# Kernel tuning notes

Hardware: AMD Instinct MI355X
Metric: run time of the kernel (lower is better)

The kernel has to match this reference:

```python
import jax, jax.numpy as jnp
import numpy as np

DIM = 384
HEADS = 8


def _dwconv3x3(x, w):
    # depthwise 3x3, groups = channels, padding=1 (SAME)
    return jax.lax.conv_general_dilated(
        x, w, window_strides=(1, 1), padding='SAME',
        feature_group_count=x.shape[1],
        dimension_numbers=('NCHW', 'OIHW', 'NCHW'))


def _conv1x1(x, w):
    return jax.lax.conv_general_dilated(
        x, w, window_strides=(1, 1), padding='SAME',
        dimension_numbers=('NCHW', 'OIHW', 'NCHW'))


def setup_inputs() -> dict:
    key = jax.random.key(0)
    ks = jax.random.split(key, 7)
    b, h, w = 2, 128, 128
    f = lambda k, s: jax.random.normal(k, s, dtype=jnp.float32)
    return {
        'k_fea': f(ks[0], (b, DIM, h, w)),
        'v_fea': f(ks[1], (b, DIM, h, w)),
        'q_fea': f(ks[2], (b, DIM, h, w)),
        'wq': f(ks[3], (DIM, 1, 3, 3)) * 0.1,
        'wk': f(ks[4], (DIM, 1, 3, 3)) * 0.1,
        'wv': f(ks[5], (DIM, 1, 3, 3)) * 0.1,
        'wproj': f(ks[6], (DIM, DIM, 1, 1)) * 0.05,
        'temperature': jnp.ones((HEADS, 1, 1), jnp.float32),
        'attn_w': jnp.full((4,), 0.2, jnp.float32),  # attn1..attn4 scalars
    }


def reference(k_fea, v_fea, q_fea, wq, wk, wv, wproj, temperature, attn_w):
    b, c, h, w = q_fea.shape
    q = _dwconv3x3(q_fea, wq)
    k = _dwconv3x3(k_fea, wk)
    v = _dwconv3x3(v_fea, wv)
    hw = h * w
    C = c // HEADS  # channels per head
    rs = lambda t: t.reshape(b, HEADS, C, hw)
    q, k, v = rs(q), rs(k), rs(v)
    # F.normalize(dim=-1): L2 normalize with eps clamp
    norm = lambda t: t / jnp.maximum(
        jnp.linalg.norm(t, axis=-1, keepdims=True), 1e-12)
    q, k = norm(q), norm(k)
    # channel-channel attention [b, heads, C, C]
    attn = jnp.einsum('bhcn,bhdn->bhcd', q, k) * temperature
    ar = jnp.arange(C)
    neg_inf = jnp.float32(-jnp.inf)
    ks_list = [C // 2, C * 2 // 3, C * 3 // 4, C * 4 // 5]
    out = jnp.zeros((b, HEADS, C, hw), attn.dtype)
    for i, topk in enumerate(ks_list):
        idx = jax.lax.top_k(attn, topk)[1]          # [b,h,C,topk]
        mask = (idx[..., None] == ar).any(axis=-2)  # [b,h,C,C] bool
        a = jax.nn.softmax(jnp.where(mask, attn, neg_inf), axis=-1)
        out = out + attn_w[i] * jnp.einsum('bhcd,bhdn->bhcn', a, v)
    out = out.reshape(b, c, h, w)
    return _conv1x1(out, wproj)
```

## Files before the change

kernel.cpp:

```cpp
#include <hip/hip_runtime.h>
#include <stdint.h>

#define NB 2
#define CH 384
#define NH 8
#define CPH 48
#define IMG 128
#define HW 16384

typedef float f32x4 __attribute__((ext_vector_type(4)));
typedef short bf16x8 __attribute__((ext_vector_type(8)));
typedef short short4v __attribute__((ext_vector_type(4)));

__device__ inline unsigned short f2bf(float f){
    unsigned u = __builtin_bit_cast(unsigned, f);
    u += 0x7FFFu + ((u >> 16) & 1u);
    return (unsigned short)(u >> 16);
}
__device__ inline float bf2f(unsigned short h){
    unsigned u = ((unsigned)h) << 16;
    return __builtin_bit_cast(float, u);
}

__device__ __forceinline__ void conv8(const float* __restrict__ pl,
                                      const float* w9, int x, int y, float* o)
{
#pragma unroll
    for (int j = 0; j < 8; ++j) o[j] = 0.f;
#pragma unroll
    for (int dy = 0; dy < 3; ++dy) {
        const int yy = y + dy - 1;
        const float vm = (yy >= 0 && yy < IMG) ? 1.f : 0.f;
        const int yc = yy < 0 ? 0 : (yy > IMG - 1 ? IMG - 1 : yy);
        const float* row = pl + yc * IMG;
        float4 A  = *(const float4*)(row + x);
        float4 Bv = *(const float4*)(row + x + 4);
        float lf = (x > 0)       ? row[x - 1] * vm : 0.f;
        float rt = (x < IMG - 8) ? row[x + 8] * vm : 0.f;
        A.x *= vm; A.y *= vm; A.z *= vm; A.w *= vm;
        Bv.x *= vm; Bv.y *= vm; Bv.z *= vm; Bv.w *= vm;
        const float a0 = w9[dy * 3], a1 = w9[dy * 3 + 1], a2 = w9[dy * 3 + 2];
        o[0] += a0 * lf   + a1 * A.x  + a2 * A.y;
        o[1] += a0 * A.x  + a1 * A.y  + a2 * A.z;
        o[2] += a0 * A.y  + a1 * A.z  + a2 * A.w;
        o[3] += a0 * A.z  + a1 * A.w  + a2 * Bv.x;
        o[4] += a0 * A.w  + a1 * Bv.x + a2 * Bv.y;
        o[5] += a0 * Bv.x + a1 * Bv.y + a2 * Bv.z;
        o[6] += a0 * Bv.y + a1 * Bv.z + a2 * Bv.w;
        o[7] += a0 * Bv.z + a1 * Bv.w + a2 * rt;
    }
}

__device__ __forceinline__ void packhl(const float* o, bf16x8& hi, bf16x8& lo,
                                       float& sq)
{
#pragma unroll
    for (int j = 0; j < 8; ++j) {
        sq += o[j] * o[j];
        unsigned short hh = f2bf(o[j]);
        hi[j] = (short)hh;
        lo[j] = (short)f2bf(o[j] - bf2f(hh));
    }
}

__global__ __launch_bounds__(256) void k_gramf(
    const float* __restrict__ qf, const float* __restrict__ kf,
    const float* __restrict__ wq, const float* __restrict__ wk,
    float* __restrict__ Sg, float* __restrict__ ssqg)
{
    __shared__ float sred[4][2304];
    __shared__ float ssr[4][96];
    const int t = threadIdx.x;
    const int s = blockIdx.x, bh = blockIdx.y;
    const int wid = t >> 6, lane = t & 63, quad = lane >> 4, l15 = lane & 15;
    const int b = bh >> 3, h = bh & 7;
    const int y = s * 4 + wid;

    const float* qpl[3];
    const float* kpl[3];
    float wqr[3][9], wkr[3][9];
#pragma unroll
    for (int i = 0; i < 3; ++i) {
        const int c = h * CPH + i * 16 + l15;
        qpl[i] = qf + (size_t)(b * CH + c) * HW;
        kpl[i] = kf + (size_t)(b * CH + c) * HW;
#pragma unroll
        for (int j = 0; j < 9; ++j) {
            wqr[i][j] = wq[c * 9 + j];
            wkr[i][j] = wk[c * 9 + j];
        }
    }

    f32x4 acc[3][3];
#pragma unroll
    for (int i = 0; i < 3; ++i)
#pragma unroll
        for (int j = 0; j < 3; ++j) acc[i][j] = (f32x4){0.f, 0.f, 0.f, 0.f};
    float sqq[3] = {0.f, 0.f, 0.f}, sqk[3] = {0.f, 0.f, 0.f};

    for (int ks = 0; ks < 4; ++ks) {
        const int x = ks * 32 + quad * 8;
        bf16x8 qh[3], ql_[3], kh[3], kl[3];
#pragma unroll
        for (int i = 0; i < 3; ++i) {
            float o[8];
            conv8(qpl[i], wqr[i], x, y, o);
            packhl(o, qh[i], ql_[i], sqq[i]);
            conv8(kpl[i], wkr[i], x, y, o);
            packhl(o, kh[i], kl[i], sqk[i]);
        }
#pragma unroll
        for (int ci = 0; ci < 3; ++ci)
#pragma unroll
            for (int di = 0; di < 3; ++di) {
                acc[ci][di] = __builtin_amdgcn_mfma_f32_16x16x32_bf16(qh[ci],  kh[di], acc[ci][di], 0, 0, 0);
                acc[ci][di] = __builtin_amdgcn_mfma_f32_16x16x32_bf16(qh[ci],  kl[di], acc[ci][di], 0, 0, 0);
                acc[ci][di] = __builtin_amdgcn_mfma_f32_16x16x32_bf16(ql_[ci], kh[di], acc[ci][di], 0, 0, 0);
            }
    }

#pragma unroll
    for (int i = 0; i < 3; ++i) {
#pragma unroll
        for (int off = 16; off <= 32; off <<= 1) {
            sqq[i] += __shfl_xor(sqq[i], off);
            sqk[i] += __shfl_xor(sqk[i], off);
        }
        if (lane < 16) {
            ssr[wid][i * 16 + l15]      = sqq[i];
            ssr[wid][48 + i * 16 + l15] = sqk[i];
        }
    }

#pragma unroll
    for (int ci = 0; ci < 3; ++ci)
#pragma unroll
        for (int di = 0; di < 3; ++di)
#pragma unroll
            for (int r = 0; r < 4; ++r)
                sred[wid][(ci * 16 + quad * 4 + r) * 48 + di * 16 + l15] = acc[ci][di][r];
    __syncthreads();

    if (t < 96)
        atomicAdd(&ssqg[(size_t)bh * 96 + t],
                  ssr[0][t] + ssr[1][t] + ssr[2][t] + ssr[3][t]);

    float* Sbh = Sg + (size_t)bh * 2304;
#pragma unroll
    for (int i = 0; i < 9; ++i) {
        int e = t * 9 + i;
        atomicAdd(&Sbh[e], sred[0][e] + sred[1][e] + sred[2][e] + sred[3][e]);
    }
}

__global__ __launch_bounds__(256) void k_conv3v(
    const float* __restrict__ vf, const float* __restrict__ wv,
    unsigned short* __restrict__ Vc)
{
    const int bc = blockIdx.x;
    const int ch = bc % CH;
    const float* plane = vf + (size_t)bc * HW;
    const float* wp9 = wv + ch * 9;
    unsigned short* oh = Vc + (size_t)bc * HW;

    float w9[9];
#pragma unroll
    for (int i = 0; i < 9; ++i) w9[i] = wp9[i];

    const int t = threadIdx.x;
    const int wvid = t >> 6, lane = t & 63;
    const int rb = lane >> 5, cx = lane & 31;

    for (int pass = 0; pass < 16; ++pass) {
        const int y = wvid * 32 + pass * 2 + rb;
        float o0 = 0.f, o1 = 0.f, o2 = 0.f, o3 = 0.f;
#pragma unroll
        for (int dy = 0; dy < 3; ++dy) {
            const int yy = y + dy - 1;
            const float vm = (yy >= 0 && yy < IMG) ? 1.f : 0.f;
            const int yc = yy < 0 ? 0 : (yy > IMG - 1 ? IMG - 1 : yy);
            float4 r4 = *(const float4*)(plane + yc * IMG + 4 * cx);
            r4.x *= vm; r4.y *= vm; r4.z *= vm; r4.w *= vm;
            float lf = __shfl(r4.w, (lane + 63) & 63);
            if (cx == 0) lf = 0.f;
            float rt = __shfl(r4.x, (lane + 1) & 63);
            if (cx == 31) rt = 0.f;
            const float a0 = w9[dy * 3], a1 = w9[dy * 3 + 1], a2 = w9[dy * 3 + 2];
            o0 += a0 * lf   + a1 * r4.x + a2 * r4.y;
            o1 += a0 * r4.x + a1 * r4.y + a2 * r4.z;
            o2 += a0 * r4.y + a1 * r4.z + a2 * r4.w;
            o3 += a0 * r4.z + a1 * r4.w + a2 * rt;
        }
        short4v pv = {(short)f2bf(o0), (short)f2bf(o1), (short)f2bf(o2), (short)f2bf(o3)};
        *(short4v*)(oh + y * IMG + 4 * cx) = pv;
    }
}

__global__ void k_attn(const float* __restrict__ Sg, const float* __restrict__ ssqg,
                       const float* __restrict__ temp, const float* __restrict__ aw,
                       float* __restrict__ Mg)
{
    const int t = threadIdx.x;
    const int r = blockIdx.x * 4 + (t >> 6);
    const int lane = t & 63;
    const int c = r % 48, h = (r / 48) % NH, b = r / (48 * NH);
    const float* Srow = Sg + ((size_t)(b * NH + h) * 48 + c) * 48;
    const float* sq = ssqg + (size_t)(b * NH + h) * 96;

    float v = -3.0e38f;
    if (lane < 48) {
        float nq = fmaxf(sqrtf(sq[c]), 1e-12f);
        float nk = fmaxf(sqrtf(sq[48 + lane]), 1e-12f);
        v = Srow[lane] / (nq * nk) * temp[h];
    }
    float m = v;
#pragma unroll
    for (int off = 32; off; off >>= 1) m = fmaxf(m, __shfl_xor(m, off));
    int rank = 0;
    for (int e = 0; e < 48; ++e) {
        float ve = __shfl(v, e);
        rank += ((ve > v) || (ve == v && e < lane)) ? 1 : 0;
    }
    float ed = (lane < 48) ? __expf(v - m) : 0.f;
    const int K4[4] = {24, 32, 36, 38};
    float f = 0.f;
#pragma unroll
    for (int i = 0; i < 4; ++i) {
        float x = (rank < K4[i]) ? ed : 0.f;
#pragma unroll
        for (int off = 32; off; off >>= 1) x += __shfl_xor(x, off);
        if (rank < K4[i]) f += aw[i] / x;
    }
    if (lane < 48) Mg[((size_t)(b * NH + h) * 48 + c) * 48 + lane] = ed * f;
}

__global__ void k_w2(const float* __restrict__ wproj, const float* __restrict__ Mg,
                     unsigned short* __restrict__ W2)
{
    int idx = blockIdx.x * 256 + threadIdx.x;
    int gd = idx % 384; int co = (idx / 384) % 384; int b = idx / (384 * 384);
    int h = gd / 48, d = gd % 48;
    const float* wp = wproj + (size_t)co * 384 + h * 48;
    const float* Mp = Mg + (size_t)(b * NH + h) * 2304 + d;
    float s = 0.f;
#pragma unroll
    for (int cc = 0; cc < 48; ++cc) s += wp[cc] * Mp[cc * 48];
    W2[idx] = f2bf(s);
}

__global__ __launch_bounds__(256) void k_trans(const unsigned short* __restrict__ Vc,
                                               unsigned short* __restrict__ Vct)
{
    __shared__ unsigned short S[64][66];
    const int nt = blockIdx.x, ct = blockIdx.y, b = blockIdx.z;
    const int t = threadIdx.x, r = t >> 2, seg = t & 3;
    const unsigned short* src = Vc + (size_t)(b * CH + ct * 64 + r) * HW + nt * 64 + seg * 16;
    *(bf16x8*)&S[r][seg * 16]     = *(const bf16x8*)src;
    *(bf16x8*)&S[r][seg * 16 + 8] = *(const bf16x8*)(src + 8);
    __syncthreads();
    unsigned short tmp[16];
#pragma unroll
    for (int i = 0; i < 16; ++i) tmp[i] = S[seg * 16 + i][r];
    unsigned short* dst = Vct + ((size_t)b * HW + nt * 64 + r) * CH + ct * 64 + seg * 16;
    *(bf16x8*)dst       = *(const bf16x8*)&tmp[0];
    *(bf16x8*)(dst + 8) = *(const bf16x8*)&tmp[8];
}

__global__ __launch_bounds__(256) void k_gemm2(const unsigned short* __restrict__ W2,
        const unsigned short* __restrict__ Vct, float* __restrict__ out)
{
    const int t = threadIdx.x;
    const int y = blockIdx.x, mt = blockIdx.y, b = blockIdx.z;
    const int wid = t >> 6, lane = t & 63, quad = lane >> 4, l15 = lane & 15;
    const int wm = wid >> 1, wn = wid & 1;

    f32x4 acc[4][4];
#pragma unroll
    for (int i = 0; i < 4; ++i)
#pragma unroll
        for (int j = 0; j < 4; ++j) acc[i][j] = (f32x4){0.f, 0.f, 0.f, 0.f};

    const unsigned short* Ab[4];
    const unsigned short* Bb[4];
#pragma unroll
    for (int i = 0; i < 4; ++i) {
        Ab[i] = W2 + (size_t)(b * CH + mt * 128 + wm * 64 + i * 16 + l15) * CH + quad * 8;
        Bb[i] = Vct + ((size_t)b * HW + y * IMG + wn * 64 + i * 16 + l15) * CH + quad * 8;
    }

    for (int kt = 0; kt < 12; ++kt) {
        const int K0 = kt * 32;
        bf16x8 af[4], bfr[4];
#pragma unroll
        for (int i = 0; i < 4; ++i) af[i]  = *(const bf16x8*)(Ab[i] + K0);
#pragma unroll
        for (int i = 0; i < 4; ++i) bfr[i] = *(const bf16x8*)(Bb[i] + K0);
#pragma unroll
        for (int mi = 0; mi < 4; ++mi)
#pragma unroll
            for (int ni = 0; ni < 4; ++ni)
                acc[mi][ni] = __builtin_amdgcn_mfma_f32_16x16x32_bf16(af[mi], bfr[ni], acc[mi][ni], 0, 0, 0);
    }
#pragma unroll
    for (int mi = 0; mi < 4; ++mi)
#pragma unroll
        for (int ni = 0; ni < 4; ++ni)
#pragma unroll
            for (int r = 0; r < 4; ++r) {
                int co = mt * 128 + wm * 64 + mi * 16 + quad * 4 + r;
                int n  = y * IMG + wn * 64 + ni * 16 + l15;
                out[(size_t)(b * CH + co) * HW + n] = acc[mi][ni][r];
            }
}

extern "C" void kernel_launch(void* const* d_in, const int* in_sizes, int n_in,
                              void* d_out, int out_size, void* d_ws, size_t ws_size,
                              hipStream_t stream)
{
    const float* k_fea = (const float*)d_in[0];
    const float* v_fea = (const float*)d_in[1];
    const float* q_fea = (const float*)d_in[2];
    const float* wq = (const float*)d_in[3];
    const float* wk = (const float*)d_in[4];
    const float* wv = (const float*)d_in[5];
    const float* wproj = (const float*)d_in[6];
    const float* temp = (const float*)d_in[7];
    const float* aw = (const float*)d_in[8];
    float* out = (float*)d_out;

    char* ws = (char*)d_ws;
    float* Sg   = (float*)ws;
    float* ssqg = (float*)(ws + 147456);
    float* Mg   = (float*)(ws + 153600);
    unsigned short* W2 = (unsigned short*)(ws + 301056);

    const size_t PLANE_BYTES = (size_t)NB * CH * HW * 2;
    unsigned short* Vc  = (unsigned short*)(ws + 890880);
    unsigned short* Vct = (unsigned short*)(ws + 890880 + PLANE_BYTES);

    hipMemsetAsync(Sg, 0, 153600, stream);
    k_conv3v<<<768, 256, 0, stream>>>(v_fea, wv, Vc);
    k_gramf<<<dim3(32, 16), 256, 0, stream>>>(q_fea, k_fea, wq, wk, Sg, ssqg);
    k_attn<<<192, 256, 0, stream>>>(Sg, ssqg, temp, aw, Mg);
    k_w2<<<1152, 256, 0, stream>>>(wproj, Mg, W2);
    k_trans<<<dim3(256, 6, 2), 256, 0, stream>>>(Vc, Vct);
    k_gemm2<<<dim3(128, 3, 2), 256, 0, stream>>>(W2, Vct, out);
}
```

Baseline: 378.6 us.

## Restructure Gram kernel to stage conv outputs in LDS with coalesced row loads

The fused q/k depthwise-conv plus Gram kernel now has each 16-lane group compute a full image row of one channel with coalesced float4 loads. Left and right halo values come from lane shuffles instead of extra scalar loads. The bf16 hi/lo results are written to XOR-swizzled shared memory and then read back in MFMA operand layout. Weights are cached in LDS, and the grid doubles to 64 blocks per head, with two rows per block and a 3-blocks-per-CU occupancy hint. The aim is better global-memory coalescing and occupancy, at the cost of extra LDS traffic, barriers per row, and twice as many atomic reductions into the Gram matrix.

```diff
diff --git a/kernel.cpp b/kernel.cpp
--- a/kernel.cpp
+++ b/kernel.cpp
@@ -22,35 +22,6 @@
     return __builtin_bit_cast(float, u);
 }
 
-__device__ __forceinline__ void conv8(const float* __restrict__ pl,
-                                      const float* w9, int x, int y, float* o)
-{
-#pragma unroll
-    for (int j = 0; j < 8; ++j) o[j] = 0.f;
-#pragma unroll
-    for (int dy = 0; dy < 3; ++dy) {
-        const int yy = y + dy - 1;
-        const float vm = (yy >= 0 && yy < IMG) ? 1.f : 0.f;
-        const int yc = yy < 0 ? 0 : (yy > IMG - 1 ? IMG - 1 : yy);
-        const float* row = pl + yc * IMG;
-        float4 A  = *(const float4*)(row + x);
-        float4 Bv = *(const float4*)(row + x + 4);
-        float lf = (x > 0)       ? row[x - 1] * vm : 0.f;
-        float rt = (x < IMG - 8) ? row[x + 8] * vm : 0.f;
-        A.x *= vm; A.y *= vm; A.z *= vm; A.w *= vm;
-        Bv.x *= vm; Bv.y *= vm; Bv.z *= vm; Bv.w *= vm;
-        const float a0 = w9[dy * 3], a1 = w9[dy * 3 + 1], a2 = w9[dy * 3 + 2];
-        o[0] += a0 * lf   + a1 * A.x  + a2 * A.y;
-        o[1] += a0 * A.x  + a1 * A.y  + a2 * A.z;
-        o[2] += a0 * A.y  + a1 * A.z  + a2 * A.w;
-        o[3] += a0 * A.z  + a1 * A.w  + a2 * Bv.x;
-        o[4] += a0 * A.w  + a1 * Bv.x + a2 * Bv.y;
-        o[5] += a0 * Bv.x + a1 * Bv.y + a2 * Bv.z;
-        o[6] += a0 * Bv.y + a1 * Bv.z + a2 * Bv.w;
-        o[7] += a0 * Bv.z + a1 * Bv.w + a2 * rt;
-    }
-}
-
 __device__ __forceinline__ void packhl(const float* o, bf16x8& hi, bf16x8& lo,
                                        float& sq)
 {
@@ -63,93 +34,129 @@
     }
 }
 
-__global__ __launch_bounds__(256) void k_gramf(
+__global__ __launch_bounds__(256, 3) void k_gramf2(
     const float* __restrict__ qf, const float* __restrict__ kf,
     const float* __restrict__ wq, const float* __restrict__ wk,
     float* __restrict__ Sg, float* __restrict__ ssqg)
 {
-    __shared__ float sred[4][2304];
-    __shared__ float ssr[4][96];
+    __shared__ char smem[49152];
+    __shared__ float ssqL[96];
+    __shared__ float wL[864];
+
     const int t = threadIdx.x;
     const int s = blockIdx.x, bh = blockIdx.y;
     const int wid = t >> 6, lane = t & 63, quad = lane >> 4, l15 = lane & 15;
     const int b = bh >> 3, h = bh & 7;
-    const int y = s * 4 + wid;
-
-    const float* qpl[3];
-    const float* kpl[3];
-    float wqr[3][9], wkr[3][9];
-#pragma unroll
-    for (int i = 0; i < 3; ++i) {
-        const int c = h * CPH + i * 16 + l15;
-        qpl[i] = qf + (size_t)(b * CH + c) * HW;
-        kpl[i] = kf + (size_t)(b * CH + c) * HW;
-#pragma unroll
-        for (int j = 0; j < 9; ++j) {
-            wqr[i][j] = wq[c * 9 + j];
-            wkr[i][j] = wk[c * 9 + j];
+
+    for (int idx = t; idx < 864; idx += 256)
+        wL[idx] = (idx < 432) ? wq[h * 432 + idx] : wk[h * 432 + idx - 432];
+    if (t < 96) ssqL[t] = 0.f;
+
+    f32x4 acc[3][3];
+#pragma unroll
+    for (int i = 0; i < 3; ++i)
+#pragma unroll
+        for (int j = 0; j < 3; ++j) acc[i][j] = (f32x4){0.f, 0.f, 0.f, 0.f};
+
+    const int xg = t & 15;
+    const int grp = t >> 4;
+
+    __syncthreads();
+
+    for (int r = 0; r < 2; ++r) {
+        const int y = s * 2 + r;
+
+#pragma unroll
+        for (int it = 0; it < 6; ++it) {
+            const int tc = it * 16 + grp;
+            const int tensor = tc >= 48 ? 1 : 0;
+            const int ch = tc - tensor * 48;
+            const float* pl = (tensor ? kf : qf) + (size_t)(b * CH + h * CPH + ch) * HW;
+            const float* wp = &wL[tensor * 432 + ch * 9];
+
+            float o[8];
+#pragma unroll
+            for (int j = 0; j < 8; ++j) o[j] = 0.f;
+#pragma unroll
+            for (int dy = 0; dy < 3; ++dy) {
+                const int yy = y + dy - 1;
+                const float vm = (yy >= 0 && yy < IMG) ? 1.f : 0.f;
+                const int yc = yy < 0 ? 0 : (yy > IMG - 1 ? IMG - 1 : yy);
+                const float* row = pl + yc * IMG + xg * 8;
+                float4 A  = *(const float4*)row;
+                float4 Bv = *(const float4*)(row + 4);
+                A.x *= vm; A.y *= vm; A.z *= vm; A.w *= vm;
+                Bv.x *= vm; Bv.y *= vm; Bv.z *= vm; Bv.w *= vm;
+                float lf = __shfl(Bv.w, (lane + 63) & 63);
+                if (xg == 0) lf = 0.f;
+                float rt = __shfl(A.x, (lane + 1) & 63);
+                if (xg == 15) rt = 0.f;
+                const float a0 = wp[dy * 3], a1 = wp[dy * 3 + 1], a2 = wp[dy * 3 + 2];
+                o[0] += a0 * lf   + a1 * A.x  + a2 * A.y;
+                o[1] += a0 * A.x  + a1 * A.y  + a2 * A.z;
+                o[2] += a0 * A.y  + a1 * A.z  + a2 * A.w;
+                o[3] += a0 * A.z  + a1 * A.w  + a2 * Bv.x;
+                o[4] += a0 * A.w  + a1 * Bv.x + a2 * Bv.y;
+                o[5] += a0 * Bv.x + a1 * Bv.y + a2 * Bv.z;
+                o[6] += a0 * Bv.y + a1 * Bv.z + a2 * Bv.w;
+                o[7] += a0 * Bv.z + a1 * Bv.w + a2 * rt;
+            }
+            float sq = 0.f;
+            bf16x8 hi, lo;
+            packhl(o, hi, lo, sq);
+#pragma unroll
+            for (int off = 1; off < 16; off <<= 1) sq += __shfl_xor(sq, off);
+            if (xg == 0) ssqL[tc] += sq;
+            const int rbase = (tensor * 96 + ch) * 256;
+            const int xb = (xg * 16) ^ ((ch & 7) << 4);
+            *(bf16x8*)(smem + rbase + xb) = hi;
+            *(bf16x8*)(smem + rbase + 48 * 256 + xb) = lo;
         }
-    }
-
-    f32x4 acc[3][3];
-#pragma unroll
-    for (int i = 0; i < 3; ++i)
-#pragma unroll
-        for (int j = 0; j < 3; ++j) acc[i][j] = (f32x4){0.f, 0.f, 0.f, 0.f};
-    float sqq[3] = {0.f, 0.f, 0.f}, sqk[3] = {0.f, 0.f, 0.f};
-
-    for (int ks = 0; ks < 4; ++ks) {
-        const int x = ks * 32 + quad * 8;
-        bf16x8 qh[3], ql_[3], kh[3], kl[3];
-#pragma unroll
-        for (int i = 0; i < 3; ++i) {
-            float o[8];
-            conv8(qpl[i], wqr[i], x, y, o);
-            packhl(o, qh[i], ql_[i], sqq[i]);
-            conv8(kpl[i], wkr[i], x, y, o);
-            packhl(o, kh[i], kl[i], sqk[i]);
+        __syncthreads();
+
+        {
+            const int koff = wid * 64 + quad * 16;
+            bf16x8 qh[3], ql_[3], kh[3], kl[3];
+#pragma unroll
+            for (int i = 0; i < 3; ++i) {
+                const int ch = i * 16 + l15;
+                const int xb = koff ^ ((ch & 7) << 4);
+                const char* base = smem + ch * 256 + xb;
+                qh[i]  = *(const bf16x8*)(base);
+                ql_[i] = *(const bf16x8*)(base + 48 * 256);
+                kh[i]  = *(const bf16x8*)(base + 96 * 256);
+                kl[i]  = *(const bf16x8*)(base + 144 * 256);
+            }
+#pragma unroll
+            for (int ci = 0; ci < 3; ++ci)
+#pragma unroll
+                for (int di = 0; di < 3; ++di) {
+                    acc[ci][di] = __builtin_amdgcn_mfma_f32_16x16x32_bf16(qh[ci],  kh[di], acc[ci][di], 0, 0, 0);
+                    acc[ci][di] = __builtin_amdgcn_mfma_f32_16x16x32_bf16(qh[ci],  kl[di], acc[ci][di], 0, 0, 0);
+                    acc[ci][di] = __builtin_amdgcn_mfma_f32_16x16x32_bf16(ql_[ci], kh[di], acc[ci][di], 0, 0, 0);
+                }
         }
-#pragma unroll
-        for (int ci = 0; ci < 3; ++ci)
-#pragma unroll
-            for (int di = 0; di < 3; ++di) {
-                acc[ci][di] = __builtin_amdgcn_mfma_f32_16x16x32_bf16(qh[ci],  kh[di], acc[ci][di], 0, 0, 0);
-                acc[ci][di] = __builtin_amdgcn_mfma_f32_16x16x32_bf16(qh[ci],  kl[di], acc[ci][di], 0, 0, 0);
-                acc[ci][di] = __builtin_amdgcn_mfma_f32_16x16x32_bf16(ql_[ci], kh[di], acc[ci][di], 0, 0, 0);
-            }
-    }
-
-#pragma unroll
-    for (int i = 0; i < 3; ++i) {
-#pragma unroll
-        for (int off = 16; off <= 32; off <<= 1) {
-            sqq[i] += __shfl_xor(sqq[i], off);
-            sqk[i] += __shfl_xor(sqk[i], off);
-        }
-        if (lane < 16) {
-            ssr[wid][i * 16 + l15]      = sqq[i];
-            ssr[wid][48 + i * 16 + l15] = sqk[i];
-        }
-    }
-
+        __syncthreads();
+    }
+
+    float* sred = (float*)smem;
 #pragma unroll
     for (int ci = 0; ci < 3; ++ci)
 #pragma unroll
         for (int di = 0; di < 3; ++di)
 #pragma unroll
             for (int r = 0; r < 4; ++r)
-                sred[wid][(ci * 16 + quad * 4 + r) * 48 + di * 16 + l15] = acc[ci][di][r];
+                sred[wid * 2304 + (ci * 16 + quad * 4 + r) * 48 + di * 16 + l15] = acc[ci][di][r];
     __syncthreads();
 
     if (t < 96)
-        atomicAdd(&ssqg[(size_t)bh * 96 + t],
-                  ssr[0][t] + ssr[1][t] + ssr[2][t] + ssr[3][t]);
+        atomicAdd(&ssqg[(size_t)bh * 96 + t], ssqL[t]);
 
     float* Sbh = Sg + (size_t)bh * 2304;
 #pragma unroll
     for (int i = 0; i < 9; ++i) {
         int e = t * 9 + i;
-        atomicAdd(&Sbh[e], sred[0][e] + sred[1][e] + sred[2][e] + sred[3][e]);
+        atomicAdd(&Sbh[e], sred[e] + sred[2304 + e] + sred[4608 + e] + sred[6912 + e]);
     }
 }
 
@@ -340,7 +347,7 @@
 
     hipMemsetAsync(Sg, 0, 153600, stream);
     k_conv3v<<<768, 256, 0, stream>>>(v_fea, wv, Vc);
-    k_gramf<<<dim3(32, 16), 256, 0, stream>>>(q_fea, k_fea, wq, wk, Sg, ssqg);
+    k_gramf2<<<dim3(64, 16), 256, 0, stream>>>(q_fea, k_fea, wq, wk, Sg, ssqg);
     k_attn<<<192, 256, 0, stream>>>(Sg, ssqg, temp, aw, Mg);
     k_w2<<<1152, 256, 0, stream>>>(wproj, Mg, W2);
     k_trans<<<dim3(256, 6, 2), 256, 0, stream>>>(Vc, Vct);
```

Result: faster. 335.2 us (-11.5%).
